# Kernel optimization log

Measured on AMD Instinct MI355X. Metric: run time of the kernel, lower is better.

Reference implementation:

```python
import jax, jax.numpy as jnp
import numpy as np

BATCH, SEQ_LEN, VEC_DIM, WIDTH = 64, 256, 512, 3


def setup_inputs() -> dict:
    key = jax.random.key(0)
    k = jax.random.split(key, 8)
    F0r = jax.random.normal(k[0], (BATCH, SEQ_LEN, VEC_DIM), jnp.float32)
    F1r = jax.random.normal(k[1], (BATCH, SEQ_LEN, VEC_DIM), jnp.float32)
    sent0_mask = (jax.random.uniform(k[2], (BATCH, SEQ_LEN)) < 0.9).astype(jnp.float32)
    sent1_mask = (jax.random.uniform(k[3], (BATCH, SEQ_LEN)) < 0.9).astype(jnp.float32)
    # nn.Parameter(torch.randn(seq_len, vec_dim))
    W0 = jax.random.normal(k[4], (SEQ_LEN, VEC_DIM), jnp.float32)
    W1 = jax.random.normal(k[5], (SEQ_LEN, VEC_DIM), jnp.float32)
    # Conv2d(2, 1, kernel_size=(WIDTH, 1)) default init: U(-1/sqrt(fan_in), +)
    bound = 1.0 / np.sqrt(2 * WIDTH * 1)
    conv_w = jax.random.uniform(k[6], (1, 2, WIDTH, 1), jnp.float32, -bound, bound)
    conv_b = jax.random.uniform(k[7], (1,), jnp.float32, -bound, bound)
    return dict(F0r=F0r, F1r=F1r, sent0_mask=sent0_mask, sent1_mask=sent1_mask,
                W0=W0, W1=W1, conv_w=conv_w, conv_b=conv_b)


def _conv_tanh_pool(x, conv_w, conv_b):
    # x: [B, 2, S, D]; conv pad (WIDTH-1, 0) -> [B, 1, S+WIDTH-1, D]
    y = jax.lax.conv_general_dilated(
        x, conv_w, window_strides=(1, 1),
        padding=((WIDTH - 1, WIDTH - 1), (0, 0)),
        dimension_numbers=('NCHW', 'OIHW', 'NCHW'))
    y = jnp.tanh(y + conv_b[None, :, None, None])
    # AvgPool2d kernel (WIDTH,1), stride 1 -> [B, 1, S, D]
    y = jax.lax.reduce_window(y, 0.0, jax.lax.add,
                              (1, 1, WIDTH, 1), (1, 1, 1, 1), 'VALID') / WIDTH
    return y[:, 0]  # squeeze channel -> [B, S, D]


def reference(F0r, F1r, sent0_mask, sent1_mask, W0, W1, conv_w, conv_b):
    # masking is in-place in the torch code, so masked F0/F1 feed the conv too
    F0 = F0r * sent0_mask[:, :, None]  # [B, S, D]
    F1 = F1r * sent1_mask[:, :, None]
    # pairwise L2 via ||u-v||^2 = ||u||^2 + ||v||^2 - 2 u.v (avoids [B,S,S,D])
    sq0 = jnp.sum(F0 * F0, axis=-1)  # [B, S]
    sq1 = jnp.sum(F1 * F1, axis=-1)
    cross = jnp.einsum('bid,bjd->bij', F0, F1)  # [B, S, S]
    d2 = jnp.maximum(sq0[:, :, None] + sq1[:, None, :] - 2.0 * cross, 0.0)
    norm = jnp.where(d2 > 0, jnp.sqrt(jnp.where(d2 > 0, d2, 1.0)), 0.0)
    A = 1.0 / (1.0 + norm)  # [B, S, S]
    F0a = jnp.einsum('bij,id->bjd', A, W0)  # A^T @ W0
    F1a = jnp.einsum('bij,jd->bid', A, W1)  # A @ W1
    x0 = jnp.stack([F0, F0a], axis=1)  # [B, 2, S, D]
    x1 = jnp.stack([F1, F1a], axis=1)
    out0 = _conv_tanh_pool(x0, conv_w, conv_b)
    out1 = _conv_tanh_pool(x1, conv_w, conv_b)
    return out0, out1
```

## Files before the change

### kernel.cpp

```cpp
#include <hip/hip_runtime.h>

typedef unsigned short u16;
typedef __attribute__((ext_vector_type(8))) short short8;
typedef __attribute__((ext_vector_type(4))) float f32x4;

__device__ inline u16 f2bf(float f) {
    union { float f; unsigned u; } v; v.f = f;
    unsigned u = v.u;
    unsigned r = (u + 0x7FFFu + ((u >> 16) & 1u)) >> 16;
    return (u16)r;
}
__device__ inline float bf2f(u16 h) {
    union { unsigned u; float f; } v; v.u = ((unsigned)h) << 16;
    return v.f;
}
__device__ inline float ftanh(float x) {
    float e = __expf(2.f * x);
    return 1.f - 2.f / (e + 1.f);
}

__global__ __launch_bounds__(128) void prep_kernel(
    const float* __restrict__ F0r, const float* __restrict__ F1r,
    const float* __restrict__ m0, const float* __restrict__ m1,
    u16* __restrict__ F0b, u16* __restrict__ F1b,
    float* __restrict__ sq0, float* __restrict__ sq1)
{
    int bs = blockIdx.x;
    int t = threadIdx.x;
    size_t base = (size_t)bs * 512 + t * 4;
    float mk0 = m0[bs], mk1 = m1[bs];
    float4 v0 = *(const float4*)(F0r + base);
    float4 v1 = *(const float4*)(F1r + base);
    v0.x *= mk0; v0.y *= mk0; v0.z *= mk0; v0.w *= mk0;
    v1.x *= mk1; v1.y *= mk1; v1.z *= mk1; v1.w *= mk1;
    ushort4 u0; u0.x = f2bf(v0.x); u0.y = f2bf(v0.y); u0.z = f2bf(v0.z); u0.w = f2bf(v0.w);
    ushort4 u1; u1.x = f2bf(v1.x); u1.y = f2bf(v1.y); u1.z = f2bf(v1.z); u1.w = f2bf(v1.w);
    *(ushort4*)(F0b + base) = u0;
    *(ushort4*)(F1b + base) = u1;
    float s0p = v0.x*v0.x + v0.y*v0.y + v0.z*v0.z + v0.w*v0.w;
    float s1p = v1.x*v1.x + v1.y*v1.y + v1.z*v1.z + v1.w*v1.w;
    #pragma unroll
    for (int off = 32; off > 0; off >>= 1) {
        s0p += __shfl_xor(s0p, off);
        s1p += __shfl_xor(s1p, off);
    }
    __shared__ float red0[2], red1[2];
    if ((t & 63) == 0) { red0[t >> 6] = s0p; red1[t >> 6] = s1p; }
    __syncthreads();
    if (t == 0) { sq0[bs] = red0[0] + red0[1]; sq1[bs] = red1[0] + red1[1]; }
}

__global__ __launch_bounds__(256) void wtrans_kernel(
    const float* __restrict__ W0, const float* __restrict__ W1,
    u16* __restrict__ WT0, u16* __restrict__ WT1)
{
    int idx = blockIdx.x * 256 + threadIdx.x;
    int a = idx >> 17;
    int r = idx & 131071;
    int s = r >> 9, d = r & 511;
    const float* W = a ? W1 : W0;
    u16* WT = a ? WT1 : WT0;
    WT[d * 256 + s] = f2bf(W[r]);
}

__device__ inline void gemm64_core(
    const u16* __restrict__ Ap, int lda,
    const u16* __restrict__ Bp, int ldb,
    int K, int m0, int n0,
    u16 (*As)[72], u16 (*Bs)[72],
    f32x4 acc[2][2])
{
    const int t = threadIdx.x;
    const int lane = t & 63, w = t >> 6;
    const int wm = w >> 1, wn = w & 1;
    const int q = lane >> 4, lm = lane & 15;
    const int srow = t >> 3;
    const int sseg = t & 7;

    for (int k0 = 0; k0 < K; k0 += 64) {
        #pragma unroll
        for (int i = 0; i < 2; ++i) {
            int row = i * 32 + srow;
            *(uint4*)&As[row][sseg * 8] =
                *(const uint4*)(Ap + (size_t)(m0 + row) * lda + k0 + sseg * 8);
            *(uint4*)&Bs[row][sseg * 8] =
                *(const uint4*)(Bp + (size_t)(n0 + row) * ldb + k0 + sseg * 8);
        }
        __syncthreads();
        #pragma unroll
        for (int ks = 0; ks < 64; ks += 32) {
            short8 af[2], bfr[2];
            #pragma unroll
            for (int x = 0; x < 2; ++x) {
                af[x]  = *(const short8*)&As[wm * 32 + x * 16 + lm][ks + q * 8];
                bfr[x] = *(const short8*)&Bs[wn * 32 + x * 16 + lm][ks + q * 8];
            }
            #pragma unroll
            for (int x = 0; x < 2; ++x)
                #pragma unroll
                for (int y = 0; y < 2; ++y)
                    acc[x][y] = __builtin_amdgcn_mfma_f32_16x16x32_bf16(
                        af[x], bfr[y], acc[x][y], 0, 0, 0);
        }
        __syncthreads();
    }
}

__global__ __launch_bounds__(256) void gemm_cross_kernel(
    const u16* __restrict__ F0b, const u16* __restrict__ F1b,
    const float* __restrict__ sq0, const float* __restrict__ sq1,
    u16* __restrict__ Abf, u16* __restrict__ ATbf)
{
    __shared__ __align__(16) u16 As[64][72];
    __shared__ __align__(16) u16 Bs[64][72];
    int b = blockIdx.y;
    int i0 = (blockIdx.x >> 2) * 64, j0 = (blockIdx.x & 3) * 64;
    const u16* Ap = F0b + (size_t)b * 131072;
    const u16* Bp = F1b + (size_t)b * 131072;
    const float* sqR = sq0 + b * 256;
    const float* sqC = sq1 + b * 256;

    f32x4 acc[2][2];
    #pragma unroll
    for (int x = 0; x < 2; ++x)
        #pragma unroll
        for (int y = 0; y < 2; ++y)
            acc[x][y] = (f32x4){0.f, 0.f, 0.f, 0.f};

    gemm64_core(Ap, 512, Bp, 512, 512, i0, j0, As, Bs, acc);

    const int t = threadIdx.x;
    const int lane = t & 63, w = t >> 6;
    const int wm = w >> 1, wn = w & 1, q = lane >> 4, lm = lane & 15;
    u16 (*Ct)[72] = As;
    #pragma unroll
    for (int x = 0; x < 2; ++x) {
        #pragma unroll
        for (int r = 0; r < 4; ++r) {
            int ir = wm * 32 + x * 16 + q * 4 + r;
            float si = sqR[i0 + ir];
            #pragma unroll
            for (int y = 0; y < 2; ++y) {
                int jc = wn * 32 + y * 16 + lm;
                float d2 = si + sqC[j0 + jc] - 2.f * acc[x][y][r];
                d2 = fmaxf(d2, 0.f);
                float a = 1.f / (1.f + sqrtf(d2));
                Ct[ir][jc] = f2bf(a);
            }
        }
    }
    __syncthreads();

    u16* Aout  = Abf  + (size_t)b * 65536;
    u16* ATout = ATbf + (size_t)b * 65536;
    int ii = t >> 2;
    int c0 = (t & 3) * 16;
    #pragma unroll
    for (int c = 0; c < 4; ++c) {
        ushort4 v = *(ushort4*)&Ct[ii][c0 + c * 4];
        *(ushort4*)&Aout[(size_t)(i0 + ii) * 256 + j0 + c0 + c * 4] = v;
    }
    #pragma unroll
    for (int c = 0; c < 4; ++c) {
        ushort4 v;
        v.x = Ct[c0 + c * 4 + 0][ii];
        v.y = Ct[c0 + c * 4 + 1][ii];
        v.z = Ct[c0 + c * 4 + 2][ii];
        v.w = Ct[c0 + c * 4 + 3][ii];
        *(ushort4*)&ATout[(size_t)(j0 + ii) * 256 + i0 + c0 + c * 4] = v;
    }
}

__global__ __launch_bounds__(256) void gemm_fa_kernel(
    const u16* __restrict__ Abf, const u16* __restrict__ ATbf,
    const u16* __restrict__ WT0, const u16* __restrict__ WT1,
    u16* __restrict__ F0a, u16* __restrict__ F1a)
{
    __shared__ __align__(16) u16 As[64][72];
    __shared__ __align__(16) u16 Bs[64][72];
    int b = blockIdx.y, var = blockIdx.z;
    int m0 = (blockIdx.x >> 3) * 64;
    int n0 = (blockIdx.x & 7) * 64;
    const u16 *Ap, *Bp; u16* Out;
    if (var == 0) { Ap = ATbf + (size_t)b * 65536; Bp = WT0; Out = F0a + (size_t)b * 131072; }
    else          { Ap = Abf  + (size_t)b * 65536; Bp = WT1; Out = F1a + (size_t)b * 131072; }

    f32x4 acc[2][2];
    #pragma unroll
    for (int x = 0; x < 2; ++x)
        #pragma unroll
        for (int y = 0; y < 2; ++y)
            acc[x][y] = (f32x4){0.f, 0.f, 0.f, 0.f};

    gemm64_core(Ap, 256, Bp, 256, 256, m0, n0, As, Bs, acc);

    const int t = threadIdx.x;
    const int lane = t & 63, w = t >> 6;
    const int wm = w >> 1, wn = w & 1, q = lane >> 4, lm = lane & 15;
    u16 (*Ct)[72] = As;
    #pragma unroll
    for (int x = 0; x < 2; ++x)
        #pragma unroll
        for (int r = 0; r < 4; ++r) {
            int ir = wm * 32 + x * 16 + q * 4 + r;
            #pragma unroll
            for (int y = 0; y < 2; ++y) {
                int jc = wn * 32 + y * 16 + lm;
                Ct[ir][jc] = f2bf(acc[x][y][r]);
            }
        }
    __syncthreads();
    int ii = t >> 2;
    int c0 = (t & 3) * 16;
    #pragma unroll
    for (int c = 0; c < 4; ++c) {
        ushort4 v = *(ushort4*)&Ct[ii][c0 + c * 4];
        *(ushort4*)&Out[(size_t)(m0 + ii) * 512 + n0 + c0 + c * 4] = v;
    }
}

__device__ inline void load_row_cv(
    const float* __restrict__ Fr, const float* __restrict__ mask,
    const u16* __restrict__ Fa, int s, int d0, float4& f, float4& a)
{
    if ((unsigned)s < 256u) {
        float4 v = *(const float4*)(Fr + (size_t)s * 512 + d0);
        float m = mask[s];
        f.x = v.x * m; f.y = v.y * m; f.z = v.z * m; f.w = v.w * m;
        ushort4 u = *(const ushort4*)(Fa + (size_t)s * 512 + d0);
        a.x = bf2f(u.x); a.y = bf2f(u.y); a.z = bf2f(u.z); a.w = bf2f(u.w);
    } else {
        f = make_float4(0.f, 0.f, 0.f, 0.f);
        a = make_float4(0.f, 0.f, 0.f, 0.f);
    }
}

__global__ __launch_bounds__(128) void conv_kernel(
    const float* __restrict__ F0r, const float* __restrict__ F1r,
    const float* __restrict__ m0, const float* __restrict__ m1,
    const u16* __restrict__ F0a, const u16* __restrict__ F1a,
    const float* __restrict__ cw, const float* __restrict__ cb,
    float* __restrict__ out)
{
    int b = blockIdx.y;
    int which = blockIdx.z;
    int s0 = blockIdx.x * 16;
    int d0 = threadIdx.x * 4;
    const float* Fr = (which ? F1r : F0r) + (size_t)b * 131072;
    const float* mask = (which ? m1 : m0) + b * 256;
    const u16* Fa = (which ? F1a : F0a) + (size_t)b * 131072;
    float* o = out + (size_t)which * 8388608 + (size_t)b * 131072 + d0;
    float w00 = cw[0], w01 = cw[1], w02 = cw[2];
    float w10 = cw[3], w11 = cw[4], w12 = cw[5];
    float bias = cb[0];

    float4 fm2, fm1, fc, fp1, fp2, am2, am1, ac, ap1, ap2;
    load_row_cv(Fr, mask, Fa, s0 - 2, d0, fm2, am2);
    load_row_cv(Fr, mask, Fa, s0 - 1, d0, fm1, am1);
    load_row_cv(Fr, mask, Fa, s0,     d0, fc,  ac);
    load_row_cv(Fr, mask, Fa, s0 + 1, d0, fp1, ap1);
    load_row_cv(Fr, mask, Fa, s0 + 2, d0, fp2, ap2);

    #define CONV_Y(Y, F0_, F1_, F2_, A0_, A1_, A2_)                                \
        { Y.x = bias + w00*F0_.x + w01*F1_.x + w02*F2_.x + w10*A0_.x + w11*A1_.x + w12*A2_.x; \
          Y.y = bias + w00*F0_.y + w01*F1_.y + w02*F2_.y + w10*A0_.y + w11*A1_.y + w12*A2_.y; \
          Y.z = bias + w00*F0_.z + w01*F1_.z + w02*F2_.z + w10*A0_.z + w11*A1_.z + w12*A2_.z; \
          Y.w = bias + w00*F0_.w + w01*F1_.w + w02*F2_.w + w10*A0_.w + w11*A1_.w + w12*A2_.w; }
    #define TANH4(Y) { Y.x = ftanh(Y.x); Y.y = ftanh(Y.y); Y.z = ftanh(Y.z); Y.w = ftanh(Y.w); }

    float4 ty0, ty1;
    CONV_Y(ty0, fm2, fm1, fc, am2, am1, ac); TANH4(ty0);
    CONV_Y(ty1, fm1, fc, fp1, am1, ac, ap1); TANH4(ty1);

    float4 w0f = fc, w1f = fp1, w2f = fp2;
    float4 w0a = ac, w1a = ap1, w2a = ap2;
    const float third = 1.f / 3.f;
    for (int s = s0; s < s0 + 16; ++s) {
        float4 ty2;
        CONV_Y(ty2, w0f, w1f, w2f, w0a, w1a, w2a); TANH4(ty2);
        float4 r;
        r.x = (ty0.x + ty1.x + ty2.x) * third;
        r.y = (ty0.y + ty1.y + ty2.y) * third;
        r.z = (ty0.z + ty1.z + ty2.z) * third;
        r.w = (ty0.w + ty1.w + ty2.w) * third;
        *(float4*)(o + (size_t)s * 512) = r;
        ty0 = ty1; ty1 = ty2;
        w0f = w1f; w1f = w2f;
        w0a = w1a; w1a = w2a;
        load_row_cv(Fr, mask, Fa, s + 3, d0, w2f, w2a);
    }
    #undef CONV_Y
    #undef TANH4
}

extern "C" void kernel_launch(void* const* d_in, const int* in_sizes, int n_in,
                              void* d_out, int out_size, void* d_ws, size_t ws_size,
                              hipStream_t stream)
{
    const float* F0r = (const float*)d_in[0];
    const float* F1r = (const float*)d_in[1];
    const float* m0  = (const float*)d_in[2];
    const float* m1  = (const float*)d_in[3];
    const float* W0  = (const float*)d_in[4];
    const float* W1  = (const float*)d_in[5];
    const float* cw  = (const float*)d_in[6];
    const float* cb  = (const float*)d_in[7];
    float* out = (float*)d_out;

    char* ws = (char*)d_ws;
    u16* F0b   = (u16*)(ws);
    u16* F1b   = (u16*)(ws + 16777216);
    u16* Abf   = (u16*)(ws + 33554432);
    u16* ATbf  = (u16*)(ws + 41943040);
    float* sq0 = (float*)(ws + 50331648);
    float* sq1 = (float*)(ws + 50397184);
    u16* WT0   = (u16*)(ws + 50462720);
    u16* WT1   = (u16*)(ws + 50724864);
    u16* F0a = F0b;
    u16* F1a = F1b;

    prep_kernel<<<16384, 128, 0, stream>>>(F0r, F1r, m0, m1, F0b, F1b, sq0, sq1);
    wtrans_kernel<<<1024, 256, 0, stream>>>(W0, W1, WT0, WT1);
    gemm_cross_kernel<<<dim3(16, 64), 256, 0, stream>>>(F0b, F1b, sq0, sq1, Abf, ATbf);
    gemm_fa_kernel<<<dim3(32, 64, 2), 256, 0, stream>>>(Abf, ATbf, WT0, WT1, F0a, F1a);
    conv_kernel<<<dim3(16, 64, 2), 128, 0, stream>>>(F0r, F1r, m0, m1, F0a, F1a, cw, cb, out);
}
```

Measured before the change: 208.3 us.

## Fuse W transpose into prep, widen GEMM tiles, conv reads bf16 masked features

Folds the W transpose into the prep kernel as extra blocks, which removes one launch. The cross GEMM now uses a K-tile of 128 and the FA GEMM uses a 64x128 output tile, so fewer blocks load the shared operands and there are fewer barriers. F0a and F1a get their own workspace buffers, so the conv kernel can read the bf16 masked features written by prep instead of the fp32 inputs and masks. This halves the conv's feature read traffic, but it lowers the precision of the conv's direct-feature path to bf16.

```diff
diff --git a/kernel.cpp b/kernel.cpp
--- a/kernel.cpp
+++ b/kernel.cpp
@@ -22,11 +22,24 @@
 __global__ __launch_bounds__(128) void prep_kernel(
     const float* __restrict__ F0r, const float* __restrict__ F1r,
     const float* __restrict__ m0, const float* __restrict__ m1,
+    const float* __restrict__ W0, const float* __restrict__ W1,
     u16* __restrict__ F0b, u16* __restrict__ F1b,
+    u16* __restrict__ WT0, u16* __restrict__ WT1,
     float* __restrict__ sq0, float* __restrict__ sq1)
 {
-    int bs = blockIdx.x;
+    int bx = blockIdx.x;
     int t = threadIdx.x;
+    if (bx >= 16384) {
+        int idx = (bx - 16384) * 128 + t;
+        int a = idx >> 17;
+        int r = idx & 131071;
+        int s = r >> 9, d = r & 511;
+        const float* W = a ? W1 : W0;
+        u16* WT = a ? WT1 : WT0;
+        WT[d * 256 + s] = f2bf(W[r]);
+        return;
+    }
+    int bs = bx;
     size_t base = (size_t)bs * 512 + t * 4;
     float mk0 = m0[bs], mk1 = m1[bs];
     float4 v0 = *(const float4*)(F0r + base);
@@ -50,69 +63,15 @@
     if (t == 0) { sq0[bs] = red0[0] + red0[1]; sq1[bs] = red1[0] + red1[1]; }
 }
 
-__global__ __launch_bounds__(256) void wtrans_kernel(
-    const float* __restrict__ W0, const float* __restrict__ W1,
-    u16* __restrict__ WT0, u16* __restrict__ WT1)
-{
-    int idx = blockIdx.x * 256 + threadIdx.x;
-    int a = idx >> 17;
-    int r = idx & 131071;
-    int s = r >> 9, d = r & 511;
-    const float* W = a ? W1 : W0;
-    u16* WT = a ? WT1 : WT0;
-    WT[d * 256 + s] = f2bf(W[r]);
-}
-
-__device__ inline void gemm64_core(
-    const u16* __restrict__ Ap, int lda,
-    const u16* __restrict__ Bp, int ldb,
-    int K, int m0, int n0,
-    u16 (*As)[72], u16 (*Bs)[72],
-    f32x4 acc[2][2])
-{
-    const int t = threadIdx.x;
-    const int lane = t & 63, w = t >> 6;
-    const int wm = w >> 1, wn = w & 1;
-    const int q = lane >> 4, lm = lane & 15;
-    const int srow = t >> 3;
-    const int sseg = t & 7;
-
-    for (int k0 = 0; k0 < K; k0 += 64) {
-        #pragma unroll
-        for (int i = 0; i < 2; ++i) {
-            int row = i * 32 + srow;
-            *(uint4*)&As[row][sseg * 8] =
-                *(const uint4*)(Ap + (size_t)(m0 + row) * lda + k0 + sseg * 8);
-            *(uint4*)&Bs[row][sseg * 8] =
-                *(const uint4*)(Bp + (size_t)(n0 + row) * ldb + k0 + sseg * 8);
-        }
-        __syncthreads();
-        #pragma unroll
-        for (int ks = 0; ks < 64; ks += 32) {
-            short8 af[2], bfr[2];
-            #pragma unroll
-            for (int x = 0; x < 2; ++x) {
-                af[x]  = *(const short8*)&As[wm * 32 + x * 16 + lm][ks + q * 8];
-                bfr[x] = *(const short8*)&Bs[wn * 32 + x * 16 + lm][ks + q * 8];
-            }
-            #pragma unroll
-            for (int x = 0; x < 2; ++x)
-                #pragma unroll
-                for (int y = 0; y < 2; ++y)
-                    acc[x][y] = __builtin_amdgcn_mfma_f32_16x16x32_bf16(
-                        af[x], bfr[y], acc[x][y], 0, 0, 0);
-        }
-        __syncthreads();
-    }
-}
-
 __global__ __launch_bounds__(256) void gemm_cross_kernel(
     const u16* __restrict__ F0b, const u16* __restrict__ F1b,
     const float* __restrict__ sq0, const float* __restrict__ sq1,
     u16* __restrict__ Abf, u16* __restrict__ ATbf)
 {
-    __shared__ __align__(16) u16 As[64][72];
-    __shared__ __align__(16) u16 Bs[64][72];
+    __shared__ __align__(16) u16 smem[64 * 136 * 2];
+    u16 (*As)[136] = (u16(*)[136])smem;
+    u16 (*Bs)[136] = (u16(*)[136])(smem + 64 * 136);
+
     int b = blockIdx.y;
     int i0 = (blockIdx.x >> 2) * 64, j0 = (blockIdx.x & 3) * 64;
     const u16* Ap = F0b + (size_t)b * 131072;
@@ -120,6 +79,11 @@
     const float* sqR = sq0 + b * 256;
     const float* sqC = sq1 + b * 256;
 
+    const int t = threadIdx.x;
+    const int lane = t & 63, w = t >> 6;
+    const int wm = w >> 1, wn = w & 1;
+    const int q = lane >> 4, lm = lane & 15;
+
     f32x4 acc[2][2];
     #pragma unroll
     for (int x = 0; x < 2; ++x)
@@ -127,12 +91,37 @@
         for (int y = 0; y < 2; ++y)
             acc[x][y] = (f32x4){0.f, 0.f, 0.f, 0.f};
 
-    gemm64_core(Ap, 512, Bp, 512, 512, i0, j0, As, Bs, acc);
-
-    const int t = threadIdx.x;
-    const int lane = t & 63, w = t >> 6;
-    const int wm = w >> 1, wn = w & 1, q = lane >> 4, lm = lane & 15;
-    u16 (*Ct)[72] = As;
+    for (int k0 = 0; k0 < 512; k0 += 128) {
+        #pragma unroll
+        for (int i = 0; i < 4; ++i) {
+            int idx = i * 256 + t;
+            int row = idx >> 4;
+            int seg = idx & 15;
+            *(uint4*)&As[row][seg * 8] =
+                *(const uint4*)(Ap + (size_t)(i0 + row) * 512 + k0 + seg * 8);
+            *(uint4*)&Bs[row][seg * 8] =
+                *(const uint4*)(Bp + (size_t)(j0 + row) * 512 + k0 + seg * 8);
+        }
+        __syncthreads();
+        #pragma unroll
+        for (int ks = 0; ks < 128; ks += 32) {
+            short8 af[2], bfr[2];
+            #pragma unroll
+            for (int x = 0; x < 2; ++x) {
+                af[x]  = *(const short8*)&As[wm * 32 + x * 16 + lm][ks + q * 8];
+                bfr[x] = *(const short8*)&Bs[wn * 32 + x * 16 + lm][ks + q * 8];
+            }
+            #pragma unroll
+            for (int x = 0; x < 2; ++x)
+                #pragma unroll
+                for (int y = 0; y < 2; ++y)
+                    acc[x][y] = __builtin_amdgcn_mfma_f32_16x16x32_bf16(
+                        af[x], bfr[y], acc[x][y], 0, 0, 0);
+        }
+        __syncthreads();
+    }
+
+    u16 (*Ct)[136] = (u16(*)[136])smem;
     #pragma unroll
     for (int x = 0; x < 2; ++x) {
         #pragma unroll
@@ -176,59 +165,94 @@
     const u16* __restrict__ WT0, const u16* __restrict__ WT1,
     u16* __restrict__ F0a, u16* __restrict__ F1a)
 {
-    __shared__ __align__(16) u16 As[64][72];
-    __shared__ __align__(16) u16 Bs[64][72];
+    __shared__ __align__(16) u16 smem[64 * 72 + 128 * 72];
+    u16 (*As)[72] = (u16(*)[72])smem;
+    u16 (*Bs)[72] = (u16(*)[72])(smem + 64 * 72);
+
     int b = blockIdx.y, var = blockIdx.z;
-    int m0 = (blockIdx.x >> 3) * 64;
-    int n0 = (blockIdx.x & 7) * 64;
+    int m0 = (blockIdx.x >> 2) * 64;
+    int n0 = (blockIdx.x & 3) * 128;
     const u16 *Ap, *Bp; u16* Out;
     if (var == 0) { Ap = ATbf + (size_t)b * 65536; Bp = WT0; Out = F0a + (size_t)b * 131072; }
     else          { Ap = Abf  + (size_t)b * 65536; Bp = WT1; Out = F1a + (size_t)b * 131072; }
 
-    f32x4 acc[2][2];
-    #pragma unroll
-    for (int x = 0; x < 2; ++x)
-        #pragma unroll
-        for (int y = 0; y < 2; ++y)
-            acc[x][y] = (f32x4){0.f, 0.f, 0.f, 0.f};
-
-    gemm64_core(Ap, 256, Bp, 256, 256, m0, n0, As, Bs, acc);
-
     const int t = threadIdx.x;
     const int lane = t & 63, w = t >> 6;
-    const int wm = w >> 1, wn = w & 1, q = lane >> 4, lm = lane & 15;
-    u16 (*Ct)[72] = As;
+    const int wm = w >> 1, wn = w & 1;
+    const int q = lane >> 4, lm = lane & 15;
+
+    f32x4 acc[2][4];
+    #pragma unroll
+    for (int x = 0; x < 2; ++x)
+        #pragma unroll
+        for (int y = 0; y < 4; ++y)
+            acc[x][y] = (f32x4){0.f, 0.f, 0.f, 0.f};
+
+    for (int k0 = 0; k0 < 256; k0 += 64) {
+        #pragma unroll
+        for (int i = 0; i < 6; ++i) {
+            int idx = i * 256 + t;
+            int row = idx >> 3;
+            int seg = idx & 7;
+            uint4 v;
+            if (row < 64)
+                v = *(const uint4*)(Ap + (size_t)(m0 + row) * 256 + k0 + seg * 8);
+            else
+                v = *(const uint4*)(Bp + (size_t)(n0 + row - 64) * 256 + k0 + seg * 8);
+            if (row < 64) *(uint4*)&As[row][seg * 8] = v;
+            else          *(uint4*)&Bs[row - 64][seg * 8] = v;
+        }
+        __syncthreads();
+        #pragma unroll
+        for (int ks = 0; ks < 64; ks += 32) {
+            short8 af[2], bfr[4];
+            #pragma unroll
+            for (int x = 0; x < 2; ++x)
+                af[x] = *(const short8*)&As[wm * 32 + x * 16 + lm][ks + q * 8];
+            #pragma unroll
+            for (int y = 0; y < 4; ++y)
+                bfr[y] = *(const short8*)&Bs[wn * 64 + y * 16 + lm][ks + q * 8];
+            #pragma unroll
+            for (int x = 0; x < 2; ++x)
+                #pragma unroll
+                for (int y = 0; y < 4; ++y)
+                    acc[x][y] = __builtin_amdgcn_mfma_f32_16x16x32_bf16(
+                        af[x], bfr[y], acc[x][y], 0, 0, 0);
+        }
+        __syncthreads();
+    }
+
+    u16 (*Ct)[136] = (u16(*)[136])smem;
     #pragma unroll
     for (int x = 0; x < 2; ++x)
         #pragma unroll
         for (int r = 0; r < 4; ++r) {
             int ir = wm * 32 + x * 16 + q * 4 + r;
             #pragma unroll
-            for (int y = 0; y < 2; ++y) {
-                int jc = wn * 32 + y * 16 + lm;
+            for (int y = 0; y < 4; ++y) {
+                int jc = wn * 64 + y * 16 + lm;
                 Ct[ir][jc] = f2bf(acc[x][y][r]);
             }
         }
     __syncthreads();
     int ii = t >> 2;
-    int c0 = (t & 3) * 16;
-    #pragma unroll
-    for (int c = 0; c < 4; ++c) {
+    int c0 = (t & 3) * 32;
+    #pragma unroll
+    for (int c = 0; c < 8; ++c) {
         ushort4 v = *(ushort4*)&Ct[ii][c0 + c * 4];
         *(ushort4*)&Out[(size_t)(m0 + ii) * 512 + n0 + c0 + c * 4] = v;
     }
 }
 
 __device__ inline void load_row_cv(
-    const float* __restrict__ Fr, const float* __restrict__ mask,
-    const u16* __restrict__ Fa, int s, int d0, float4& f, float4& a)
+    const u16* __restrict__ Fb, const u16* __restrict__ Fa,
+    int s, int d0, float4& f, float4& a)
 {
     if ((unsigned)s < 256u) {
-        float4 v = *(const float4*)(Fr + (size_t)s * 512 + d0);
-        float m = mask[s];
-        f.x = v.x * m; f.y = v.y * m; f.z = v.z * m; f.w = v.w * m;
-        ushort4 u = *(const ushort4*)(Fa + (size_t)s * 512 + d0);
-        a.x = bf2f(u.x); a.y = bf2f(u.y); a.z = bf2f(u.z); a.w = bf2f(u.w);
+        ushort4 uf = *(const ushort4*)(Fb + (size_t)s * 512 + d0);
+        ushort4 ua = *(const ushort4*)(Fa + (size_t)s * 512 + d0);
+        f.x = bf2f(uf.x); f.y = bf2f(uf.y); f.z = bf2f(uf.z); f.w = bf2f(uf.w);
+        a.x = bf2f(ua.x); a.y = bf2f(ua.y); a.z = bf2f(ua.z); a.w = bf2f(ua.w);
     } else {
         f = make_float4(0.f, 0.f, 0.f, 0.f);
         a = make_float4(0.f, 0.f, 0.f, 0.f);
@@ -236,8 +260,7 @@
 }
 
 __global__ __launch_bounds__(128) void conv_kernel(
-    const float* __restrict__ F0r, const float* __restrict__ F1r,
-    const float* __restrict__ m0, const float* __restrict__ m1,
+    const u16* __restrict__ F0b, const u16* __restrict__ F1b,
     const u16* __restrict__ F0a, const u16* __restrict__ F1a,
     const float* __restrict__ cw, const float* __restrict__ cb,
     float* __restrict__ out)
@@ -246,8 +269,7 @@
     int which = blockIdx.z;
     int s0 = blockIdx.x * 16;
     int d0 = threadIdx.x * 4;
-    const float* Fr = (which ? F1r : F0r) + (size_t)b * 131072;
-    const float* mask = (which ? m1 : m0) + b * 256;
+    const u16* Fb = (which ? F1b : F0b) + (size_t)b * 131072;
     const u16* Fa = (which ? F1a : F0a) + (size_t)b * 131072;
     float* o = out + (size_t)which * 8388608 + (size_t)b * 131072 + d0;
     float w00 = cw[0], w01 = cw[1], w02 = cw[2];
@@ -255,11 +277,11 @@
     float bias = cb[0];
 
     float4 fm2, fm1, fc, fp1, fp2, am2, am1, ac, ap1, ap2;
-    load_row_cv(Fr, mask, Fa, s0 - 2, d0, fm2, am2);
-    load_row_cv(Fr, mask, Fa, s0 - 1, d0, fm1, am1);
-    load_row_cv(Fr, mask, Fa, s0,     d0, fc,  ac);
-    load_row_cv(Fr, mask, Fa, s0 + 1, d0, fp1, ap1);
-    load_row_cv(Fr, mask, Fa, s0 + 2, d0, fp2, ap2);
+    load_row_cv(Fb, Fa, s0 - 2, d0, fm2, am2);
+    load_row_cv(Fb, Fa, s0 - 1, d0, fm1, am1);
+    load_row_cv(Fb, Fa, s0,     d0, fc,  ac);
+    load_row_cv(Fb, Fa, s0 + 1, d0, fp1, ap1);
+    load_row_cv(Fb, Fa, s0 + 2, d0, fp2, ap2);
 
     #define CONV_Y(Y, F0_, F1_, F2_, A0_, A1_, A2_)                                \
         { Y.x = bias + w00*F0_.x + w01*F1_.x + w02*F2_.x + w10*A0_.x + w11*A1_.x + w12*A2_.x; \
@@ -287,7 +309,7 @@
         ty0 = ty1; ty1 = ty2;
         w0f = w1f; w1f = w2f;
         w0a = w1a; w1a = w2a;
-        load_row_cv(Fr, mask, Fa, s + 3, d0, w2f, w2a);
+        load_row_cv(Fb, Fa, s + 3, d0, w2f, w2a);
     }
     #undef CONV_Y
     #undef TANH4
@@ -310,18 +332,18 @@
     char* ws = (char*)d_ws;
     u16* F0b   = (u16*)(ws);
     u16* F1b   = (u16*)(ws + 16777216);
-    u16* Abf   = (u16*)(ws + 33554432);
-    u16* ATbf  = (u16*)(ws + 41943040);
-    float* sq0 = (float*)(ws + 50331648);
-    float* sq1 = (float*)(ws + 50397184);
-    u16* WT0   = (u16*)(ws + 50462720);
-    u16* WT1   = (u16*)(ws + 50724864);
-    u16* F0a = F0b;
-    u16* F1a = F1b;
-
-    prep_kernel<<<16384, 128, 0, stream>>>(F0r, F1r, m0, m1, F0b, F1b, sq0, sq1);
-    wtrans_kernel<<<1024, 256, 0, stream>>>(W0, W1, WT0, WT1);
+    u16* F0a   = (u16*)(ws + 33554432);
+    u16* F1a   = (u16*)(ws + 50331648);
+    u16* Abf   = (u16*)(ws + 67108864);
+    u16* ATbf  = (u16*)(ws + 75497472);
+    float* sq0 = (float*)(ws + 83886080);
+    float* sq1 = (float*)(ws + 83951616);
+    u16* WT0   = (u16*)(ws + 84017152);
+    u16* WT1   = (u16*)(ws + 84279296);
+
+    prep_kernel<<<18432, 128, 0, stream>>>(F0r, F1r, m0, m1, W0, W1,
+                                           F0b, F1b, WT0, WT1, sq0, sq1);
     gemm_cross_kernel<<<dim3(16, 64), 256, 0, stream>>>(F0b, F1b, sq0, sq1, Abf, ATbf);
-    gemm_fa_kernel<<<dim3(32, 64, 2), 256, 0, stream>>>(Abf, ATbf, WT0, WT1, F0a, F1a);
-    conv_kernel<<<dim3(16, 64, 2), 128, 0, stream>>>(F0r, F1r, m0, m1, F0a, F1a, cw, cb, out);
-}
+    gemm_fa_kernel<<<dim3(16, 64, 2), 256, 0, stream>>>(Abf, ATbf, WT0, WT1, F0a, F1a);
+    conv_kernel<<<dim3(16, 64, 2), 128, 0, stream>>>(F0b, F1b, F0a, F1a, cw, cb, out);
+}
```

Result: no change. 210.5 us (+1.1%).
